# Kernel tuning notes

Measured on AMD Instinct MI355X. Metric: run time of the kernel, lower is better.

## Reference

```python
import jax, jax.numpy as jnp
import numpy as np
from jax import lax

SCORE_THR = 0.1
IOU_THR = 0.3
NUM_CLASSES = 80
MAX_COORD = 4096.0  # class offset for class-aware NMS (boxes live in [0, ~1100])


def setup_inputs() -> dict:
    key = jax.random.key(0)
    bs, n = 4, 4096
    k1, k2, k3, k4 = jax.random.split(key, 4)
    # realistic boxes: centers in [0,1024], w/h in [10,210]
    cxcy = jax.random.uniform(k1, (bs, n, 2), minval=0.0, maxval=1024.0)
    wh = jax.random.uniform(k2, (bs, n, 2), minval=10.0, maxval=210.0)
    x1y1 = cxcy - wh * 0.5
    x2y2 = cxcy + wh * 0.5
    scores = jax.random.uniform(k3, (bs, n, 1), minval=0.0, maxval=1.0)
    cls = jax.random.randint(k4, (bs, n, 1), 0, NUM_CLASSES).astype(jnp.float32)
    batch_preds = jnp.concatenate([x1y1, x2y2, scores, cls], axis=-1)  # [bs, n, 6]
    return {"batch_preds": batch_preds}


def _iou_matrix(boxes):
    # boxes: [N, 4] (x1, y1, x2, y2) -> pairwise IoU [N, N]
    x1, y1, x2, y2 = boxes[:, 0], boxes[:, 1], boxes[:, 2], boxes[:, 3]
    area = (x2 - x1) * (y2 - y1)
    ix1 = jnp.maximum(x1[:, None], x1[None, :])
    iy1 = jnp.maximum(y1[:, None], y1[None, :])
    ix2 = jnp.minimum(x2[:, None], x2[None, :])
    iy2 = jnp.minimum(y2[:, None], y2[None, :])
    inter = jnp.maximum(ix2 - ix1, 0.0) * jnp.maximum(iy2 - iy1, 0.0)
    return inter / (area[:, None] + area[None, :] - inter + 1e-9)


def _nms_image(preds):
    # preds: [N, 6]. Returns preds zeroed where not kept (fixed-shape mask NMS).
    n = preds.shape[0]
    boxes, scores, cls = preds[:, :4], preds[:, 4], preds[:, 5]
    valid = scores >= SCORE_THR
    # class-aware trick == per-class NMS: offset boxes by class so cross-class IoU = 0
    obox = boxes + (cls * MAX_COORD)[:, None]
    order = jnp.argsort(-jnp.where(valid, scores, -jnp.inf))
    sboxes = obox[order]
    svalid = valid[order]
    iou = _iou_matrix(sboxes)  # [N, N]
    idxs = jnp.arange(n)

    def body(suppressed, inp):
        iou_row, v_i, i = inp
        keep_i = v_i & jnp.logical_not(suppressed[i])
        suppressed = suppressed | (keep_i & (iou_row > IOU_THR) & (idxs > i))
        return suppressed, keep_i

    _, keep_sorted = lax.scan(body, jnp.zeros((n,), bool), (iou, svalid, idxs))
    keep = jnp.zeros((n,), bool).at[order].set(keep_sorted)
    return preds * keep[:, None].astype(preds.dtype)


def reference(batch_preds):
    # Fixed-shape formulation of score filtering + per-class greedy NMS:
    # suppressed / below-threshold rows are zeroed instead of removed.
    return jax.vmap(_nms_image)(batch_preds)
```

## Files before the change

kernel.cpp:

```cpp
#include <hip/hip_runtime.h>
#include <hip/hip_bf16.h>

typedef unsigned long long u64;

#define BS 4
#define NBOX 4096
#define NCLS 80
#define CPB 16
#define NBLK 5
#define SLICE 820
#define CAPC 128
#define SCORE_THR 0.1f
#define IOU_THR 0.3f
#define MAX_COORD 4096.0f

__global__ __launch_bounds__(1024) void k_nms_all(const float* __restrict__ preds,
                                                  float* __restrict__ out) {
    __shared__ unsigned mem[CPB][CAPC];
    __shared__ unsigned scnt[CPB];
    __shared__ u64 skey[CPB][CAPC];
    __shared__ float4 sbxs[CPB][CAPC];
    __shared__ unsigned sidxs[CPB][CAPC];

    const int img = blockIdx.y;
    const int g = blockIdx.x;
    const int t = threadIdx.x;
    const int w = t >> 6;
    const int lane = t & 63;
    const float* P = preds + (size_t)img * NBOX * 6;
    float* O = out + (size_t)img * NBOX * 6;

    if (t < CPB) scnt[t] = 0;
    __syncthreads();

    const int sbeg = g * SLICE;
    const int send = min(NBOX, sbeg + SLICE);
#pragma unroll
    for (int r = 0; r < NBOX / 1024; ++r) {
        int m = t + r * 1024;
        float2 sc = *(const float2*)(P + (size_t)m * 6 + 4);
        if (sc.x >= SCORE_THR) {
            int lc = (int)sc.y - g * CPB;
            if (lc >= 0 && lc < CPB) {
                unsigned slot = atomicAdd(&scnt[lc], 1u);
                if (slot < CAPC) mem[lc][slot] = (unsigned)m;
            }
        } else if (m >= sbeg && m < send) {
            float* W = O + (size_t)m * 6;
#pragma unroll
            for (int q = 0; q < 6; ++q) W[q] = 0.0f;
        }
    }
    __syncthreads();

    const int s = (int)min(scnt[w], (unsigned)CAPC);

    u64 key[2];
    float4 bx2[2] = {make_float4(0,0,0,0), make_float4(0,0,0,0)};
    unsigned oi[2] = {0, 0};
#pragma unroll
    for (int r = 0; r < 2; ++r) {
        int m = lane + 64 * r;
        key[r] = ~0ull;
        if (m < s) {
            unsigned e = mem[w][m];
            oi[r] = e;
            const float* R = P + (size_t)e * 6;
            float x1 = R[0], y1 = R[1], x2 = R[2], y2 = R[3], sc = R[4], cl = R[5];
            float off = cl * MAX_COORD;
            bx2[r] = make_float4(x1 + off, y1 + off, x2 + off, y2 + off);
            unsigned u = __float_as_uint(sc);
            u = (u & 0x80000000u) ? ~u : (u | 0x80000000u);
            key[r] = ((u64)(~u) << 32) | (u64)e;
        }
        skey[w][m] = key[r];
    }
    __syncthreads();

    int rank[2] = {0, 0};
    for (int j = 0; j < s; ++j) {
        u64 kj = skey[w][j];
        rank[0] += (kj < key[0]);
        rank[1] += (kj < key[1]);
    }
    __syncthreads();
#pragma unroll
    for (int r = 0; r < 2; ++r) {
        int m = lane + 64 * r;
        if (m < s) { sbxs[w][rank[r]] = bx2[r]; sidxs[w][rank[r]] = oi[r]; }
    }
    __syncthreads();

    float4 cb[2];
    float ca[2];
    bool removed[2];
#pragma unroll
    for (int r = 0; r < 2; ++r) {
        int c = lane + 64 * r;
        removed[r] = (c >= s);
        cb[r] = make_float4(0.f, 0.f, 0.f, 0.f);
        ca[r] = 0.f;
        if (c < s) {
            cb[r] = sbxs[w][c];
            ca[r] = (cb[r].z - cb[r].x) * (cb[r].w - cb[r].y);
        }
    }
    for (int i = 0; i < s; ++i) {
        float4 rb = sbxs[w][i];
        u64 mA = __ballot(removed[0]);
        u64 mB = __ballot(removed[1]);
        u64 m = (i < 64) ? mA : mB;
        bool kept = !((m >> (i & 63)) & 1ull);
        if (kept) {
            float ra = (rb.z - rb.x) * (rb.w - rb.y);
#pragma unroll
            for (int r = 0; r < 2; ++r) {
                int c = lane + 64 * r;
                if (c > i && !removed[r]) {
                    float ix1 = fmaxf(rb.x, cb[r].x), iy1 = fmaxf(rb.y, cb[r].y);
                    float ix2 = fminf(rb.z, cb[r].z), iy2 = fminf(rb.w, cb[r].w);
                    float iw = fmaxf(ix2 - ix1, 0.f), ih = fmaxf(iy2 - iy1, 0.f);
                    float inter = iw * ih;
                    float iou = inter / (ra + ca[r] - inter + 1e-9f);
                    if (iou > IOU_THR) removed[r] = true;
                }
            }
        }
    }

#pragma unroll
    for (int r = 0; r < 2; ++r) {
        int c = lane + 64 * r;
        if (c < s) {
            unsigned e = sidxs[w][c];
            const float* R = P + (size_t)e * 6;
            float* W = O + (size_t)e * 6;
            if (!removed[r]) {
#pragma unroll
                for (int q = 0; q < 6; ++q) W[q] = R[q];
            } else {
#pragma unroll
                for (int q = 0; q < 6; ++q) W[q] = 0.0f;
            }
        }
    }
}

extern "C" void kernel_launch(void* const* d_in, const int* in_sizes, int n_in,
                              void* d_out, int out_size, void* d_ws, size_t ws_size,
                              hipStream_t stream) {
    const float* preds = (const float*)d_in[0];
    float* out = (float*)d_out;
    k_nms_all<<<dim3(NBLK, BS), 1024, 0, stream>>>(preds, out);
}
```

Measured before the change: 75.06 us.

## Split NMS into branchless IoU bitmask build and scalar chained suppression resolve

The serial greedy loop, which ballots and branches on each kept box, is replaced by two phases. The first computes a full IoU suppression bitmask row per sorted box with no data-dependent branching. The second resolves the greedy keep set through readlane-based bit chaining over 64-bit masks. The rank loop also now runs over a fixed CAPC trip count with unrolling. This removes per-iteration ballot dependencies and divergence, at the cost of computing IoU for every pair and a long sequence of readlane operations.

```diff
diff --git a/kernel.cpp b/kernel.cpp
--- a/kernel.cpp
+++ b/kernel.cpp
@@ -13,6 +13,36 @@
 #define SCORE_THR 0.1f
 #define IOU_THR 0.3f
 #define MAX_COORD 4096.0f
+
+__device__ __forceinline__ u64 chain64(u64 dg, u64 ent) {
+    unsigned dlo = (unsigned)dg, dhi = (unsigned)(dg >> 32);
+    unsigned dA[32];
+#pragma unroll
+    for (int v = 0; v < 32; ++v)
+        dA[v] = (unsigned)__builtin_amdgcn_readlane((int)dlo, v);
+    unsigned curA = (unsigned)ent;
+#pragma unroll
+    for (int v = 0; v < 32; ++v)
+        curA |= (((curA >> v) & 1u) ? 0u : dA[v]);
+    unsigned kwA = ~curA;
+    __builtin_amdgcn_sched_barrier(0);
+    unsigned accB = 0;
+#pragma unroll
+    for (int v = 0; v < 32; ++v) {
+        unsigned hv = (unsigned)__builtin_amdgcn_readlane((int)dhi, v);
+        accB |= (((kwA >> v) & 1u) ? hv : 0u);
+    }
+    __builtin_amdgcn_sched_barrier(0);
+    unsigned dB[32];
+#pragma unroll
+    for (int v = 0; v < 32; ++v)
+        dB[v] = (unsigned)__builtin_amdgcn_readlane((int)dhi, 32 + v);
+    unsigned curB = (unsigned)(ent >> 32) | accB;
+#pragma unroll
+    for (int v = 0; v < 32; ++v)
+        curB |= (((curB >> v) & 1u) ? 0u : dB[v]);
+    return ((u64)(~curB) << 32) | (u64)kwA;
+}
 
 __global__ __launch_bounds__(1024) void k_nms_all(const float* __restrict__ preds,
                                                   float* __restrict__ out) {
@@ -77,27 +107,23 @@
     }
     __syncthreads();
 
-    int rank[2] = {0, 0};
-    for (int j = 0; j < s; ++j) {
+    int rank0 = 0, rank1 = 0;
+#pragma unroll 8
+    for (int j = 0; j < CAPC; ++j) {
         u64 kj = skey[w][j];
-        rank[0] += (kj < key[0]);
-        rank[1] += (kj < key[1]);
-    }
-    __syncthreads();
-#pragma unroll
-    for (int r = 0; r < 2; ++r) {
-        int m = lane + 64 * r;
-        if (m < s) { sbxs[w][rank[r]] = bx2[r]; sidxs[w][rank[r]] = oi[r]; }
-    }
+        rank0 += (kj < key[0]);
+        rank1 += (kj < key[1]);
+    }
+    __syncthreads();
+    if (lane < s)      { sbxs[w][rank0] = bx2[0]; sidxs[w][rank0] = oi[0]; }
+    if (lane + 64 < s) { sbxs[w][rank1] = bx2[1]; sidxs[w][rank1] = oi[1]; }
     __syncthreads();
 
     float4 cb[2];
     float ca[2];
-    bool removed[2];
 #pragma unroll
     for (int r = 0; r < 2; ++r) {
         int c = lane + 64 * r;
-        removed[r] = (c >= s);
         cb[r] = make_float4(0.f, 0.f, 0.f, 0.f);
         ca[r] = 0.f;
         if (c < s) {
@@ -105,37 +131,64 @@
             ca[r] = (cb[r].z - cb[r].x) * (cb[r].w - cb[r].y);
         }
     }
+
+    u64 rowA = 0, rowB = 0, rowB2 = 0;
     for (int i = 0; i < s; ++i) {
         float4 rb = sbxs[w][i];
-        u64 mA = __ballot(removed[0]);
-        u64 mB = __ballot(removed[1]);
-        u64 m = (i < 64) ? mA : mB;
-        bool kept = !((m >> (i & 63)) & 1ull);
-        if (kept) {
-            float ra = (rb.z - rb.x) * (rb.w - rb.y);
-#pragma unroll
-            for (int r = 0; r < 2; ++r) {
-                int c = lane + 64 * r;
-                if (c > i && !removed[r]) {
-                    float ix1 = fmaxf(rb.x, cb[r].x), iy1 = fmaxf(rb.y, cb[r].y);
-                    float ix2 = fminf(rb.z, cb[r].z), iy2 = fminf(rb.w, cb[r].w);
-                    float iw = fmaxf(ix2 - ix1, 0.f), ih = fmaxf(iy2 - iy1, 0.f);
-                    float inter = iw * ih;
-                    float iou = inter / (ra + ca[r] - inter + 1e-9f);
-                    if (iou > IOU_THR) removed[r] = true;
-                }
-            }
-        }
+        float ra = (rb.z - rb.x) * (rb.w - rb.y);
+        bool c1;
+        {
+            float ix1 = fmaxf(rb.x, cb[1].x), iy1 = fmaxf(rb.y, cb[1].y);
+            float ix2 = fminf(rb.z, cb[1].z), iy2 = fminf(rb.w, cb[1].w);
+            float iw = fmaxf(ix2 - ix1, 0.f), ih = fmaxf(iy2 - iy1, 0.f);
+            float inter = iw * ih;
+            float iou = inter / (ra + ca[1] - inter + 1e-9f);
+            c1 = ((lane + 64) > i) && (iou > IOU_THR);
+        }
+        u64 bB = __ballot(c1);
+        if (i < 64) {
+            bool c0;
+            float ix1 = fmaxf(rb.x, cb[0].x), iy1 = fmaxf(rb.y, cb[0].y);
+            float ix2 = fminf(rb.z, cb[0].z), iy2 = fminf(rb.w, cb[0].w);
+            float iw = fmaxf(ix2 - ix1, 0.f), ih = fmaxf(iy2 - iy1, 0.f);
+            float inter = iw * ih;
+            float iou = inter / (ra + ca[0] - inter + 1e-9f);
+            c0 = (lane > i) && (iou > IOU_THR);
+            u64 bA = __ballot(c0);
+            if (lane == i) { rowA = bA; rowB = bB; }
+        } else {
+            if (lane == i - 64) rowB2 = bB;
+        }
+    }
+
+    const u64 entA = (s >= 64) ? 0ull : (~0ull << s);
+    u64 kwA64 = chain64(rowA, entA);
+    u64 kwB64 = 0;
+    if (s > 64) {
+        unsigned rlo = (unsigned)rowB, rhi = (unsigned)(rowB >> 32);
+        unsigned aLo = 0, aHi = 0;
+#pragma unroll
+        for (int v = 0; v < 64; ++v) {
+            unsigned lo = (unsigned)__builtin_amdgcn_readlane((int)rlo, v);
+            unsigned hi = (unsigned)__builtin_amdgcn_readlane((int)rhi, v);
+            unsigned keep = (unsigned)((kwA64 >> v) & 1ull);
+            aLo |= keep ? lo : 0u;
+            aHi |= keep ? hi : 0u;
+        }
+        const int sb = s - 64;
+        u64 padB = (sb >= 64) ? 0ull : (~0ull << sb);
+        kwB64 = chain64(rowB2, padB | (((u64)aHi << 32) | (u64)aLo));
     }
 
 #pragma unroll
     for (int r = 0; r < 2; ++r) {
         int c = lane + 64 * r;
         if (c < s) {
+            bool kept = (((r == 0) ? kwA64 : kwB64) >> lane) & 1ull;
             unsigned e = sidxs[w][c];
             const float* R = P + (size_t)e * 6;
             float* W = O + (size_t)e * 6;
-            if (!removed[r]) {
+            if (kept) {
 #pragma unroll
                 for (int q = 0; q < 6; ++q) W[q] = R[q];
             } else {
```

Result: slower. 85.96 us (+14.5%).
